# Kernel optimization log

Hardware: AMD Instinct MI355X
Metric: run time of the kernel (lower is better)

The kernel has to match this reference:

```python
import jax, jax.numpy as jnp
import numpy as np

CLAMP_MAX = float(np.log(100.0))  # temperature clamp from MoELayer


def setup_inputs() -> dict:
    key = jax.random.key(0)
    ks = jax.random.split(key, 4)
    N, D, H, E = 524288, 128, 512, 8
    x = jax.random.normal(ks[0], (N, D), dtype=jnp.float32)
    # per-expert MLP params, stacked along expert axis; scaled like torch Linear init
    W1 = jax.random.normal(ks[1], (E, D, H), dtype=jnp.float32) / np.sqrt(D)
    b1 = jnp.zeros((E, H), dtype=jnp.float32)
    W2 = jax.random.normal(ks[2], (E, H, D), dtype=jnp.float32) / np.sqrt(H)
    b2 = jnp.zeros((E, D), dtype=jnp.float32)
    temperature = jnp.full((1,), np.log(2.0), dtype=jnp.float32)  # init from MoELayer
    return {"x": x, "W1": W1, "b1": b1, "W2": W2, "b2": b2,
            "temperature": temperature}


def reference(x, W1, b1, W2, b2, temperature):
    # Pretraining proportional router: tokens split into E contiguous equal
    # chunks (route_prob == 1), so dispatch/combine is a reshape.
    E = W1.shape[0]
    N, D = x.shape
    xe = x.reshape(E, N // E, D)                      # [E, n, D] dispatched tokens
    h = jax.nn.relu(jnp.einsum('end,edh->enh', xe, W1) + b1[:, None, :])
    y = jnp.einsum('enh,ehd->end', h, W2) + b2[:, None, :]
    logit_scale = jnp.exp(jnp.minimum(temperature, CLAMP_MAX))  # scalar [1]
    out = y.reshape(N, D) * logit_scale
    return out
```

## Files before the change

kernel.cpp:

```cpp
#include <hip/hip_runtime.h>


#define CLAMP_MAXV 4.605170185988091f

typedef __attribute__((ext_vector_type(8))) short s16x8;
typedef __attribute__((ext_vector_type(4))) float f32x4;
typedef __attribute__((ext_vector_type(4))) unsigned short u16x4;
typedef __attribute__((ext_vector_type(8))) unsigned short u16x8;

static __device__ __forceinline__ unsigned short f2bf(float f) {
  union { float f; unsigned int u; } v; v.f = f;
  unsigned int r = v.u + 0x7FFFu + ((v.u >> 16) & 1u);
  return (unsigned short)(r >> 16);
}

static __device__ __forceinline__ void gll16(const void* src, void* dst) {
  __builtin_amdgcn_global_load_lds((const __attribute__((address_space(1))) void*)src,
                                   (__attribute__((address_space(3))) void*)dst, 16, 0, 0);
}

#define LBAR() do { \
  asm volatile("s_waitcnt lgkmcnt(0)" ::: "memory"); \
  __builtin_amdgcn_s_barrier(); \
  __builtin_amdgcn_sched_barrier(0); \
} while (0)

__global__ void conv_w(const float* __restrict__ W1, const float* __restrict__ W2,
                       unsigned short* __restrict__ w1t, unsigned short* __restrict__ w2t) {
  int idx = blockIdx.x * 256 + threadIdx.x;
  if (idx < 65536) {
    int h  = idx & 511;
    int d0 = ((idx >> 9) & 15) << 3;
    int e  = idx >> 13;
    const float* src = W1 + ((size_t)e << 16);
    u16x8 v;
#pragma unroll
    for (int j = 0; j < 8; ++j) v[j] = f2bf(src[(size_t)(d0 + j) * 512 + h]);
    *(u16x8*)(w1t + ((((size_t)e << 9) + h) << 7) + d0) = v;
  } else {
    int i2 = idx - 65536;
    int d  = i2 & 127;
    int h0 = ((i2 >> 7) & 63) << 3;
    int e  = i2 >> 13;
    const float* src = W2 + ((size_t)e << 16);
    u16x8 v;
#pragma unroll
    for (int j = 0; j < 8; ++j) v[j] = f2bf(src[(size_t)(h0 + j) * 128 + d]);
    *(u16x8*)(w2t + ((((size_t)e << 7) + d) << 9) + h0) = v;
  }
}

__global__ __launch_bounds__(512, 2) void moe_fused(
    const float* __restrict__ x,
    const float* __restrict__ b1,
    const float* __restrict__ b2,
    const float* __restrict__ temp,
    const unsigned short* __restrict__ w1t,
    const unsigned short* __restrict__ w2t,
    float* __restrict__ out)
{
  __shared__ __align__(16) char smem[149504];
  char* const w1s  = smem;
  char* const hsb0 = smem + 131072;
  char* const hsb1 = smem + 139264;
  char* const xs   = smem + 131072;
  float* const b1s = (float*)(smem + 147456);

  const int tid  = threadIdx.x;
  const int lane = tid & 63;
  const int wid  = tid >> 6;
  const int l15  = lane & 15;
  const int lg   = lane >> 4;
  const int blk  = blockIdx.x;
  const int e     = blk >> 7;
  const int bslot = blk & 127;

  const unsigned short* w1g = w1t + ((size_t)e << 16);
  const unsigned short* w2g = w2t + ((size_t)e << 16);

#pragma unroll
  for (int k = 0; k < 16; ++k) {
    int s = tid + (k << 9);
    int h = s >> 4, sr = s & 15;
    gll16(w1g + ((size_t)h << 7) + ((sr ^ (h & 7)) << 3), w1s + (s << 4));
  }

  const int dlane = (wid << 4) + l15;
  s16x8 w2f[8][2];
#pragma unroll
  for (int c = 0; c < 8; ++c)
#pragma unroll
    for (int ks = 0; ks < 2; ++ks)
      w2f[c][ks] = *(const s16x8*)(w2g + ((size_t)dlane << 9) + (c << 6) + (ks << 5) + (lg << 3));

  b1s[tid] = b1[(e << 9) + tid];
  const float b2v   = b2[(e << 7) + dlane];
  const float scale = expf(fminf(temp[0], CLAMP_MAXV));

  const float* xbase = x + (((size_t)e << 16) + ((size_t)bslot << 9)) * 128 / 128 * 128;
  const float* xb0   = x + ((((size_t)e << 16) + ((size_t)bslot << 9)) << 7) / 128;
  const float* xg = x + (((size_t)(e << 16) + ((size_t)bslot << 9)) << 7) / 128;
  (void)xbase; (void)xb0; (void)xg;
  const size_t tok0 = ((size_t)e << 16) + ((size_t)bslot << 9);
  const float* xblk = x + (tok0 << 7);
  float* const oblk = out + (tok0 << 7);

  f32x4 xv[4];
#pragma unroll
  for (int it = 0; it < 4; ++it)
    xv[it] = *(const f32x4*)(xblk + ((tid + (it << 9)) << 2));

  __syncthreads();

  const int hr  = wid & 3;
  const int tq0 = (wid >> 2) << 5;
  const unsigned hl2 = (unsigned)(((hr << 4) + (lg << 2)) << 1);

#pragma unroll 1
  for (int t = 0; t < 8; ++t) {
#pragma unroll
    for (int it = 0; it < 4; ++it) {
      int idx = (tid + (it << 9)) << 2;
      int tk = idx >> 7, col = idx & 127;
      unsigned addr = (unsigned)((tk << 8) + (col << 1)) ^ (unsigned)((tk & 7) << 4);
      u16x4 p;
      p[0] = f2bf(xv[it][0]); p[1] = f2bf(xv[it][1]);
      p[2] = f2bf(xv[it][2]); p[3] = f2bf(xv[it][3]);
      *(u16x4*)(xs + addr) = p;
    }
    if (t < 7) {
      const float* xn = xblk + (((size_t)t + 1) << 13);
#pragma unroll
      for (int it = 0; it < 4; ++it)
        xv[it] = *(const f32x4*)(xn + ((tid + (it << 9)) << 2));
    }
    LBAR();

    s16x8 xb[2][4];
#pragma unroll
    for (int j = 0; j < 2; ++j) {
      int tk = tq0 + (j << 4) + l15;
#pragma unroll
      for (int ks = 0; ks < 4; ++ks) {
        unsigned koff = (unsigned)(((ks << 5) + (lg << 3)) << 1);
        xb[j][ks] = *(const s16x8*)(xs + (((unsigned)(tk << 8) + koff) ^ (unsigned)((tk & 7) << 4)));
      }
    }
    LBAR();

    f32x4 acc2[4];
#pragma unroll
    for (int i = 0; i < 4; ++i) acc2[i] = (f32x4){0.f, 0.f, 0.f, 0.f};

#pragma unroll
    for (int c = 0; c <= 8; ++c) {
      if (c < 8) {
        const int hrow = (c << 6) + (hr << 4) + l15;
        const unsigned hswz = (unsigned)((hrow & 7) << 4);
        s16x8 a[4];
#pragma unroll
        for (int ks = 0; ks < 4; ++ks) {
          unsigned koff = (unsigned)(((ks << 5) + (lg << 3)) << 1);
          a[ks] = *(const s16x8*)(w1s + (((unsigned)(hrow << 8) + koff) ^ hswz));
        }
        f32x4 acc1[2];
        acc1[0] = (f32x4){0.f, 0.f, 0.f, 0.f};
        acc1[1] = (f32x4){0.f, 0.f, 0.f, 0.f};
#pragma unroll
        for (int j = 0; j < 2; ++j)
#pragma unroll
          for (int ks = 0; ks < 4; ++ks)
            acc1[j] = __builtin_amdgcn_mfma_f32_16x16x32_bf16(a[ks], xb[j][ks], acc1[j], 0, 0, 0);

        f32x4 bias = *(const f32x4*)(b1s + (c << 6) + (hr << 4) + (lg << 2));
        char* const hw = (c & 1) ? hsb1 : hsb0;
#pragma unroll
        for (int j = 0; j < 2; ++j) {
          int tk = tq0 + (j << 4) + l15;
          u16x4 p;
#pragma unroll
          for (int r = 0; r < 4; ++r)
            p[r] = f2bf(fmaxf(acc1[j][r] + bias[r], 0.f));
          *(u16x4*)(hw + (((unsigned)(tk << 7) + hl2) ^ (unsigned)((tk & 7) << 4))) = p;
        }
      }
      if (c > 0) {
        char* const hrd = ((c - 1) & 1) ? hsb1 : hsb0;
#pragma unroll
        for (int i = 0; i < 4; ++i) {
          int tk = (i << 4) + l15;
          unsigned tswz = (unsigned)((tk & 7) << 4);
#pragma unroll
          for (int ks = 0; ks < 2; ++ks) {
            unsigned koff = (unsigned)(((ks << 5) + (lg << 3)) << 1);
            s16x8 ha = *(const s16x8*)(hrd + (((unsigned)(tk << 7) + koff) ^ tswz));
            acc2[i] = __builtin_amdgcn_mfma_f32_16x16x32_bf16(ha, w2f[c - 1][ks], acc2[i], 0, 0, 0);
          }
        }
      }
      LBAR();
    }

    float* og = oblk + ((size_t)t << 13);
#pragma unroll
    for (int i = 0; i < 4; ++i) {
#pragma unroll
      for (int r = 0; r < 4; ++r) {
        int tk = (i << 4) + (lg << 2) + r;
        og[((size_t)tk << 7) + dlane] = (acc2[i][r] + b2v) * scale;
      }
    }
  }
}

__global__ void moe_naive(const float* __restrict__ x, const float* __restrict__ W1,
                          const float* __restrict__ b1, const float* __restrict__ W2,
                          const float* __restrict__ b2, const float* __restrict__ temp,
                          float* __restrict__ out) {
  __shared__ float xr[128];
  __shared__ float hrow[512];
  int t = blockIdx.x;
  int e = t >> 16;
  int tx = threadIdx.x;
  xr[tx] = x[((size_t)t << 7) + tx];
  __syncthreads();
  const float* w1e = W1 + ((size_t)e << 16);
  for (int h = tx; h < 512; h += 128) {
    float s = b1[(e << 9) + h];
    for (int d = 0; d < 128; ++d) s += xr[d] * w1e[(size_t)d * 512 + h];
    hrow[h] = fmaxf(s, 0.f);
  }
  __syncthreads();
  const float* w2e = W2 + ((size_t)e << 16);
  float s = b2[(e << 7) + tx];
  for (int h = 0; h < 512; ++h) s += hrow[h] * w2e[(size_t)h * 128 + tx];
  out[((size_t)t << 7) + tx] = s * expf(fminf(temp[0], CLAMP_MAXV));
}

extern "C" void kernel_launch(void* const* d_in, const int* in_sizes, int n_in,
                              void* d_out, int out_size, void* d_ws, size_t ws_size,
                              hipStream_t stream) {
  const float* x    = (const float*)d_in[0];
  const float* W1   = (const float*)d_in[1];
  const float* b1   = (const float*)d_in[2];
  const float* W2   = (const float*)d_in[3];
  const float* b2   = (const float*)d_in[4];
  const float* temp = (const float*)d_in[5];
  float* out = (float*)d_out;

  const size_t WS_NEEDED = 2u * 524288u * sizeof(unsigned short);
  if (ws_size >= WS_NEEDED) {
    unsigned short* w1t = (unsigned short*)d_ws;
    unsigned short* w2t = w1t + 524288;
    conv_w<<<512, 256, 0, stream>>>(W1, W2, w1t, w2t);
    moe_fused<<<1024, 512, 0, stream>>>(x, b1, b2, temp, w1t, w2t, out);
  } else {
    moe_naive<<<524288, 128, 0, stream>>>(x, W1, b1, W2, b2, temp, out);
  }
}
```

Baseline: 193.6 us.

## Split fused MoE block into producer and consumer warp groups

```diff
diff --git a/kernel.cpp b/kernel.cpp
--- a/kernel.cpp
+++ b/kernel.cpp
@@ -50,7 +50,7 @@
   }
 }
 
-__global__ __launch_bounds__(512, 2) void moe_fused(
+__global__ __launch_bounds__(1024, 4) void moe_fused(
     const float* __restrict__ x,
     const float* __restrict__ b1,
     const float* __restrict__ b2,
@@ -59,12 +59,11 @@
     const unsigned short* __restrict__ w2t,
     float* __restrict__ out)
 {
-  __shared__ __align__(16) char smem[149504];
+  __shared__ __align__(16) char smem[147456];
   char* const w1s  = smem;
   char* const hsb0 = smem + 131072;
   char* const hsb1 = smem + 139264;
   char* const xs   = smem + 131072;
-  float* const b1s = (float*)(smem + 147456);
 
   const int tid  = threadIdx.x;
   const int lane = tid & 63;
@@ -72,142 +71,160 @@
   const int l15  = lane & 15;
   const int lg   = lane >> 4;
   const int blk  = blockIdx.x;
-  const int e     = blk >> 7;
-  const int bslot = blk & 127;
+  const int e    = blk >> 6;
+  const size_t tok0 = (size_t)blk << 10;
 
   const unsigned short* w1g = w1t + ((size_t)e << 16);
   const unsigned short* w2g = w2t + ((size_t)e << 16);
-
-#pragma unroll
-  for (int k = 0; k < 16; ++k) {
-    int s = tid + (k << 9);
+  const float* xblk = x + (tok0 << 7);
+  float* const oblk = out + (tok0 << 7);
+
+#pragma unroll
+  for (int k = 0; k < 8; ++k) {
+    int s = tid + (k << 10);
     int h = s >> 4, sr = s & 15;
     gll16(w1g + ((size_t)h << 7) + ((sr ^ (h & 7)) << 3), w1s + (s << 4));
   }
 
-  const int dlane = (wid << 4) + l15;
-  s16x8 w2f[8][2];
-#pragma unroll
-  for (int c = 0; c < 8; ++c)
-#pragma unroll
-    for (int ks = 0; ks < 2; ++ks)
-      w2f[c][ks] = *(const s16x8*)(w2g + ((size_t)dlane << 9) + (c << 6) + (ks << 5) + (lg << 3));
-
-  b1s[tid] = b1[(e << 9) + tid];
-  const float b2v   = b2[(e << 7) + dlane];
-  const float scale = expf(fminf(temp[0], CLAMP_MAXV));
-
-  const float* xbase = x + (((size_t)e << 16) + ((size_t)bslot << 9)) * 128 / 128 * 128;
-  const float* xb0   = x + ((((size_t)e << 16) + ((size_t)bslot << 9)) << 7) / 128;
-  const float* xg = x + (((size_t)(e << 16) + ((size_t)bslot << 9)) << 7) / 128;
-  (void)xbase; (void)xb0; (void)xg;
-  const size_t tok0 = ((size_t)e << 16) + ((size_t)bslot << 9);
-  const float* xblk = x + (tok0 << 7);
-  float* const oblk = out + (tok0 << 7);
-
-  f32x4 xv[4];
-#pragma unroll
-  for (int it = 0; it < 4; ++it)
-    xv[it] = *(const f32x4*)(xblk + ((tid + (it << 9)) << 2));
+  f32x4 xv[2];
+  xv[0] = *(const f32x4*)(xblk + (tid << 3));
+  xv[1] = *(const f32x4*)(xblk + (tid << 3) + 4);
 
   __syncthreads();
 
-  const int hr  = wid & 3;
-  const int tq0 = (wid >> 2) << 5;
-  const unsigned hl2 = (unsigned)(((hr << 4) + (lg << 2)) << 1);
-
-#pragma unroll 1
-  for (int t = 0; t < 8; ++t) {
-#pragma unroll
-    for (int it = 0; it < 4; ++it) {
-      int idx = (tid + (it << 9)) << 2;
-      int tk = idx >> 7, col = idx & 127;
-      unsigned addr = (unsigned)((tk << 8) + (col << 1)) ^ (unsigned)((tk & 7) << 4);
-      u16x4 p;
-      p[0] = f2bf(xv[it][0]); p[1] = f2bf(xv[it][1]);
-      p[2] = f2bf(xv[it][2]); p[3] = f2bf(xv[it][3]);
-      *(u16x4*)(xs + addr) = p;
+  const int xtok = tid >> 4;
+  const unsigned xaddr = (unsigned)((xtok << 8) + ((tid & 15) << 4)) ^ (unsigned)((xtok & 7) << 4);
+
+  if (wid < 8) {
+    const int hr  = wid & 3;
+    const int tq0 = (wid >> 2) << 5;
+    const unsigned hl2 = (unsigned)(((hr << 4) + (lg << 2)) << 1);
+
+    f32x4 bias[8];
+    const float* b1e = b1 + (e << 9);
+#pragma unroll
+    for (int c = 0; c < 8; ++c)
+      bias[c] = *(const f32x4*)(b1e + (c << 6) + (hr << 4) + (lg << 2));
+
+#pragma unroll 1
+    for (int t = 0; t < 16; ++t) {
+      u16x8 p;
+#pragma unroll
+      for (int i = 0; i < 8; ++i) p[i] = f2bf(xv[i >> 2][i & 3]);
+      *(u16x8*)(xs + xaddr) = p;
+      LBAR();
+
+      s16x8 xb[2][4];
+#pragma unroll
+      for (int j = 0; j < 2; ++j) {
+        int tk = tq0 + (j << 4) + l15;
+#pragma unroll
+        for (int ks = 0; ks < 4; ++ks) {
+          unsigned koff = (unsigned)((ks << 6) + (lg << 4));
+          xb[j][ks] = *(const s16x8*)(xs + (((unsigned)(tk << 8) + koff) ^ (unsigned)((tk & 7) << 4)));
+        }
+      }
+      LBAR();
+
+#pragma unroll 1
+      for (int c = 0; c <= 8; ++c) {
+        if (c < 8) {
+          const int hrow = (c << 6) + (hr << 4) + l15;
+          const unsigned hswz = (unsigned)((hrow & 7) << 4);
+          s16x8 a[4];
+#pragma unroll
+          for (int ks = 0; ks < 4; ++ks) {
+            unsigned koff = (unsigned)((ks << 6) + (lg << 4));
+            a[ks] = *(const s16x8*)(w1s + (((unsigned)(hrow << 8) + koff) ^ hswz));
+          }
+          f32x4 acc1[2];
+          acc1[0] = (f32x4){0.f, 0.f, 0.f, 0.f};
+          acc1[1] = (f32x4){0.f, 0.f, 0.f, 0.f};
+#pragma unroll
+          for (int j = 0; j < 2; ++j)
+#pragma unroll
+            for (int ks = 0; ks < 4; ++ks)
+              acc1[j] = __builtin_amdgcn_mfma_f32_16x16x32_bf16(a[ks], xb[j][ks], acc1[j], 0, 0, 0);
+
+          char* const hw = (c & 1) ? hsb1 : hsb0;
+#pragma unroll
+          for (int j = 0; j < 2; ++j) {
+            int tk = tq0 + (j << 4) + l15;
+            u16x4 q;
+#pragma unroll
+            for (int r = 0; r < 4; ++r)
+              q[r] = f2bf(fmaxf(acc1[j][r] + bias[c][r], 0.f));
+            *(u16x4*)(hw + (((unsigned)(tk << 7) + hl2) ^ (unsigned)((tk & 7) << 4))) = q;
+          }
+        }
+        if (c == 4 && t < 15) {
+          const float* xn = xblk + (((size_t)t + 1) << 13);
+          xv[0] = *(const f32x4*)(xn + (tid << 3));
+          xv[1] = *(const f32x4*)(xn + (tid << 3) + 4);
+        }
+        LBAR();
+      }
     }
-    if (t < 7) {
-      const float* xn = xblk + (((size_t)t + 1) << 13);
-#pragma unroll
-      for (int it = 0; it < 4; ++it)
-        xv[it] = *(const f32x4*)(xn + ((tid + (it << 9)) << 2));
-    }
-    LBAR();
-
-    s16x8 xb[2][4];
-#pragma unroll
-    for (int j = 0; j < 2; ++j) {
-      int tk = tq0 + (j << 4) + l15;
-#pragma unroll
-      for (int ks = 0; ks < 4; ++ks) {
-        unsigned koff = (unsigned)(((ks << 5) + (lg << 3)) << 1);
-        xb[j][ks] = *(const s16x8*)(xs + (((unsigned)(tk << 8) + koff) ^ (unsigned)((tk & 7) << 4)));
-      }
-    }
-    LBAR();
-
-    f32x4 acc2[4];
-#pragma unroll
-    for (int i = 0; i < 4; ++i) acc2[i] = (f32x4){0.f, 0.f, 0.f, 0.f};
-
-#pragma unroll
-    for (int c = 0; c <= 8; ++c) {
-      if (c < 8) {
-        const int hrow = (c << 6) + (hr << 4) + l15;
-        const unsigned hswz = (unsigned)((hrow & 7) << 4);
-        s16x8 a[4];
-#pragma unroll
-        for (int ks = 0; ks < 4; ++ks) {
-          unsigned koff = (unsigned)(((ks << 5) + (lg << 3)) << 1);
-          a[ks] = *(const s16x8*)(w1s + (((unsigned)(hrow << 8) + koff) ^ hswz));
-        }
-        f32x4 acc1[2];
-        acc1[0] = (f32x4){0.f, 0.f, 0.f, 0.f};
-        acc1[1] = (f32x4){0.f, 0.f, 0.f, 0.f};
-#pragma unroll
-        for (int j = 0; j < 2; ++j)
-#pragma unroll
-          for (int ks = 0; ks < 4; ++ks)
-            acc1[j] = __builtin_amdgcn_mfma_f32_16x16x32_bf16(a[ks], xb[j][ks], acc1[j], 0, 0, 0);
-
-        f32x4 bias = *(const f32x4*)(b1s + (c << 6) + (hr << 4) + (lg << 2));
-        char* const hw = (c & 1) ? hsb1 : hsb0;
-#pragma unroll
-        for (int j = 0; j < 2; ++j) {
-          int tk = tq0 + (j << 4) + l15;
-          u16x4 p;
-#pragma unroll
-          for (int r = 0; r < 4; ++r)
-            p[r] = f2bf(fmaxf(acc1[j][r] + bias[r], 0.f));
-          *(u16x4*)(hw + (((unsigned)(tk << 7) + hl2) ^ (unsigned)((tk & 7) << 4))) = p;
-        }
-      }
-      if (c > 0) {
-        char* const hrd = ((c - 1) & 1) ? hsb1 : hsb0;
-#pragma unroll
-        for (int i = 0; i < 4; ++i) {
-          int tk = (i << 4) + l15;
-          unsigned tswz = (unsigned)((tk & 7) << 4);
-#pragma unroll
-          for (int ks = 0; ks < 2; ++ks) {
-            unsigned koff = (unsigned)(((ks << 5) + (lg << 3)) << 1);
-            s16x8 ha = *(const s16x8*)(hrd + (((unsigned)(tk << 7) + koff) ^ tswz));
-            acc2[i] = __builtin_amdgcn_mfma_f32_16x16x32_bf16(ha, w2f[c - 1][ks], acc2[i], 0, 0, 0);
+  } else {
+    const int cw = wid - 8;
+    const int dlane = (cw << 4) + l15;
+
+    s16x8 w2f[8][2];
+#pragma unroll
+    for (int c = 0; c < 8; ++c)
+#pragma unroll
+      for (int ks = 0; ks < 2; ++ks)
+        w2f[c][ks] = *(const s16x8*)(w2g + ((size_t)dlane << 9) + (c << 6) + (ks << 5) + (lg << 3));
+
+    const float b2v   = b2[(e << 7) + dlane];
+    const float scale = expf(fminf(temp[0], CLAMP_MAXV));
+
+#pragma unroll 1
+    for (int t = 0; t < 16; ++t) {
+      u16x8 p;
+#pragma unroll
+      for (int i = 0; i < 8; ++i) p[i] = f2bf(xv[i >> 2][i & 3]);
+      *(u16x8*)(xs + xaddr) = p;
+      LBAR();
+      LBAR();
+
+      f32x4 acc2[4];
+#pragma unroll
+      for (int i = 0; i < 4; ++i) acc2[i] = (f32x4){0.f, 0.f, 0.f, 0.f};
+
+#pragma unroll 1
+      for (int c = 0; c <= 8; ++c) {
+        if (c >= 1) {
+          const int cc = c - 1;
+          char* const hrd = (cc & 1) ? hsb1 : hsb0;
+#pragma unroll
+          for (int i = 0; i < 4; ++i) {
+            int tk = (i << 4) + l15;
+            unsigned tswz = (unsigned)((tk & 7) << 4);
+#pragma unroll
+            for (int ks = 0; ks < 2; ++ks) {
+              unsigned koff = (unsigned)((ks << 6) + (lg << 4));
+              s16x8 ha = *(const s16x8*)(hrd + (((unsigned)(tk << 7) + koff) ^ tswz));
+              acc2[i] = __builtin_amdgcn_mfma_f32_16x16x32_bf16(ha, w2f[cc][ks], acc2[i], 0, 0, 0);
+            }
           }
         }
-      }
-      LBAR();
-    }
-
-    float* og = oblk + ((size_t)t << 13);
-#pragma unroll
-    for (int i = 0; i < 4; ++i) {
-#pragma unroll
-      for (int r = 0; r < 4; ++r) {
-        int tk = (i << 4) + (lg << 2) + r;
-        og[((size_t)tk << 7) + dlane] = (acc2[i][r] + b2v) * scale;
+        if (c == 4 && t < 15) {
+          const float* xn = xblk + (((size_t)t + 1) << 13);
+          xv[0] = *(const f32x4*)(xn + (tid << 3));
+          xv[1] = *(const f32x4*)(xn + (tid << 3) + 4);
+        }
+        LBAR();
+      }
+
+      float* og = oblk + ((size_t)t << 13);
+#pragma unroll
+      for (int i = 0; i < 4; ++i) {
+#pragma unroll
+        for (int r = 0; r < 4; ++r) {
+          int tk = (i << 4) + (lg << 2) + r;
+          og[((size_t)tk << 7) + dlane] = (acc2[i][r] + b2v) * scale;
+        }
       }
     }
   }
@@ -253,7 +270,7 @@
     unsigned short* w1t = (unsigned short*)d_ws;
     unsigned short* w2t = w1t + 524288;
     conv_w<<<512, 256, 0, stream>>>(W1, W2, w1t, w2t);
-    moe_fused<<<1024, 512, 0, stream>>>(x, b1, b2, temp, w1t, w2t, out);
+    moe_fused<<<512, 1024, 0, stream>>>(x, b1, b2, temp, w1t, w2t, out);
   } else {
     moe_naive<<<524288, 128, 0, stream>>>(x, W1, b1, W2, b2, temp, out);
   }
```

Result: slower. 392.2 us (+102.6%).
